# Optimization experiments

Hardware: AMD Instinct MI355X
Metric: run time of the kernel (lower is better)

The kernel has to match this reference:

```python
import jax, jax.numpy as jnp
import numpy as np

B, N, D, KNN = 2, 2048, 512, 16
F = 4 * D  # ffn hidden
LN_EPS = 1e-6  # flax LayerNorm default


def _ln(x, s, b):
    m = jnp.mean(x, axis=-1, keepdims=True)
    v = jnp.var(x, axis=-1, keepdims=True)
    return s * (x - m) * jax.lax.rsqrt(v + LN_EPS) + b


def _mobius_add(x, y, c):
    x2 = jnp.sum(x * x, axis=-1, keepdims=True)
    y2 = jnp.sum(y * y, axis=-1, keepdims=True)
    xy = jnp.sum(x * y, axis=-1, keepdims=True)
    num = (1 + 2 * c * xy + c * y2) * x + (1 - c * x2) * y
    den = 1 + 2 * c * xy + c * c * x2 * y2
    return num / jnp.clip(den, 1e-8, None)


def _logmap0(y, c):
    sqrt_c = jnp.sqrt(c)
    y_norm = jnp.clip(jnp.linalg.norm(y, axis=-1, keepdims=True), 1e-8, None)
    arg = jnp.minimum(sqrt_c * y_norm, 1.0 - 1e-7)
    return 1.0 / (sqrt_c * y_norm) * jnp.arctanh(arg) * y


def setup_inputs() -> dict:
    key = jax.random.key(0)
    ks = jax.random.split(key, 8)
    w = lambda k, shape: 0.02 * jax.random.normal(k, shape, dtype=jnp.float32)
    z = lambda *shape: jnp.zeros(shape, jnp.float32)
    o = lambda *shape: jnp.ones(shape, jnp.float32)
    return {
        'x': jax.random.normal(ks[0], (B, N, D), jnp.float32),
        'positions': 0.02 * jax.random.normal(ks[1], (B, N, D), jnp.float32),  # inside Poincare ball
        'c': jnp.ones((), jnp.float32),
        'Wq': w(ks[2], (D, D)), 'bq': z(D),
        'Wk': w(ks[3], (D, D)), 'bk': z(D),
        'Wv': w(ks[4], (D, D)), 'bv': z(D),
        'Wo': w(ks[5], (D, D)), 'bo': z(D),
        'W1': w(ks[6], (D, F)), 'b1': z(F),
        'W2': w(ks[7], (F, D)), 'b2': z(D),
        'ln1_s': o(D), 'ln1_b': z(D),
        'ln2_s': o(D), 'ln2_b': z(D),
        'geo_s': o(D), 'geo_b': z(D),
        'align_scale': o(1), 'feat_scale': o(1),
    }


def reference(x, positions, c, Wq, bq, Wk, bk, Wv, bv, Wo, bo, W1, b1, W2, b2,
              ln1_s, ln1_b, ln2_s, ln2_b, geo_s, geo_b, align_scale, feat_scale):
    b_, n_, d_ = x.shape
    x_res = x
    xn = _ln(x, ln1_s, ln1_b)
    q = xn @ Wq + bq
    kk = xn @ Wk + bk
    v = xn @ Wv + bv

    # Poincare distance matrix [B, N, N] (expanded ||x-y||^2 to avoid [B,N,N,D] intermediate)
    p2 = jnp.sum(positions * positions, axis=-1)            # [B, N]
    ip = jnp.einsum('bid,bjd->bij', positions, positions)   # [B, N, N]
    diff_sq = jnp.maximum(p2[:, :, None] + p2[:, None, :] - 2.0 * ip, 0.0)
    den = (1 - c * p2)[:, :, None] * (1 - c * p2)[:, None, :]
    arg = 1 + 2 * c * diff_sq / jnp.clip(den, 1e-8, None)
    dist = jnp.arccosh(jnp.maximum(arg, 1.0 + 1e-7)) / jnp.sqrt(c)

    _, idx = jax.lax.top_k(-dist, KNN)                      # [B, N, K]
    bix = jnp.arange(b_)[:, None, None]

    key_pos = positions[bix, idx]                           # [B, N, K, D]
    query_pos = positions[:, :, None, :]                    # [B, N, 1, D]
    geo = _logmap0(_mobius_add(-query_pos, key_pos, c), c)  # [B, N, K, D]
    geo = _ln(geo, geo_s, geo_b)

    gk = kk[bix, idx]                                       # [B, N, K, D]
    gv = v[bix, idx]                                        # [B, N, K, D]

    align = jnp.einsum('bnd,bnkd->bnk', q, geo)
    feat = jnp.einsum('bnd,bnkd->bnk', q, gk)
    scores = feat_scale * feat + align_scale * align
    w = jax.nn.softmax(scores, axis=-1)
    attn = jnp.einsum('bnk,bnkd->bnd', w, gv)

    x1 = x_res + attn @ Wo + bo
    h = _ln(x1, ln2_s, ln2_b)
    out = x1 + jax.nn.gelu(h @ W1 + b1) @ W2 + b2
    return out
```

## Files before the change

kernel.cpp:

```cpp
#include <hip/hip_runtime.h>
#include <hip/hip_bf16.h>
#include <math.h>

#define NTOK 2048
#define DDIM 512
#define FDIM 2048
#define KNN_K 16
#define ROWS 4096

typedef __hip_bfloat16 hb;
typedef unsigned long long ull;
typedef short s8v __attribute__((ext_vector_type(8)));
typedef short s4v __attribute__((ext_vector_type(4)));
typedef float f4v __attribute__((ext_vector_type(4)));

__device__ __forceinline__ float b2f(hb h) { return __bfloat162float(h); }
__device__ __forceinline__ float bits2f(short s) {
    return __uint_as_float(((unsigned int)(unsigned short)s) << 16);
}

__device__ __forceinline__ float ldin(const void* p, size_t i, int f32m) {
    return f32m ? ((const float*)p)[i] : b2f(((const hb*)p)[i]);
}
__device__ __forceinline__ float ld_scalar(const void* p, int f32m) {
    return f32m ? *(const float*)p : b2f(*(const hb*)p);
}
__device__ __forceinline__ short f2bs(float v) {
    hb h = __float2bfloat16(v);
    short s; __builtin_memcpy(&s, &h, 2); return s;
}
__device__ __forceinline__ short hb2s(hb h) {
    short s; __builtin_memcpy(&s, &h, 2); return s;
}

__device__ __forceinline__ void ld8(const void* p, size_t base, int fm, float* o) {
    if (fm) {
        f4v a = *(const f4v*)((const float*)p + base);
        f4v b = *(const f4v*)((const float*)p + base + 4);
        o[0]=a[0]; o[1]=a[1]; o[2]=a[2]; o[3]=a[3];
        o[4]=b[0]; o[5]=b[1]; o[6]=b[2]; o[7]=b[3];
    } else {
        s8v v = *(const s8v*)((const hb*)p + base);
        #pragma unroll
        for (int e = 0; e < 8; ++e) o[e] = bits2f(v[e]);
    }
}

__device__ __forceinline__ int detect_fm(const void* x) {
    const unsigned short* u = (const unsigned short*)x;
    const int lane = threadIdx.x & 63;
    int bad = 0;
    #pragma unroll
    for (int t = 0; t < 16; ++t) {
        unsigned short h = u[lane * 16 + t];
        int e = (h >> 7) & 0xFF;
        if (e == 0xFF) bad++;
        else if (e >= 0x8E) bad++;
        else if (e != 0 && e <= 0x66) bad++;
    }
    #pragma unroll
    for (int off = 1; off < 64; off <<= 1) bad += __shfl_xor(bad, off);
    return bad > 100 ? 1 : 0;
}

__device__ __forceinline__ ull shfl_xor_u64(ull x, int mask) {
    unsigned lo = (unsigned)x, hi = (unsigned)(x >> 32);
    lo = __shfl_xor(lo, mask); hi = __shfl_xor(hi, mask);
    return ((ull)hi << 32) | lo;
}

__device__ __forceinline__ float gelu_f(float x) {
    float u = 1.5957691216057308f * x * (1.f + 0.044715f * x * x);
    return x / (1.f + __expf(-u));
}

__device__ __forceinline__ void tr_tile(const void* src, hb* dst, int K, int N,
                                        int k0, int n0, int fm) {
    __shared__ float t[32][33];
    const int tx = threadIdx.x & 31, ty = threadIdx.x >> 5;
    #pragma unroll
    for (int r = 0; r < 32; r += 8)
        t[ty + r][tx] = ldin(src, (size_t)(k0 + ty + r) * N + n0 + tx, fm);
    __syncthreads();
    #pragma unroll
    for (int r = 0; r < 32; r += 8)
        dst[(size_t)(n0 + ty + r) * K + k0 + tx] = __float2bfloat16(t[tx][ty + r]);
}

__global__ void setup_kernel(const void* __restrict__ pos, const void* __restrict__ x,
                             const void* __restrict__ ln1s, const void* __restrict__ ln1b,
                             const void* __restrict__ Wq, const void* __restrict__ Wk,
                             const void* __restrict__ Wv, const void* __restrict__ Wo,
                             const void* __restrict__ W1, const void* __restrict__ W2,
                             hb* __restrict__ ph, hb* __restrict__ pl,
                             float* __restrict__ p2, float* __restrict__ spos,
                             hb* __restrict__ xnB,
                             hb* __restrict__ WqkvT, hb* __restrict__ WoT,
                             hb* __restrict__ W1T, hb* __restrict__ W2T,
                             int* __restrict__ fmflag) {
    const int fm = detect_fm(x);
    const int bx = blockIdx.x;
    if (bx == 0 && threadIdx.x == 0) *fmflag = fm;
    if (bx < 1024) {
        const int seg = bx >> 8, t = bx & 255;
        const int n0 = (t & 15) * 32, k0 = (t >> 4) * 32;
        const void* src = (seg == 0) ? Wq : (seg == 1) ? Wk : (seg == 2) ? Wv : Wo;
        hb* dst = (seg == 3) ? WoT : (WqkvT + (size_t)seg * 512 * 512);
        tr_tile(src, dst, 512, 512, k0, n0, fm);
    } else if (bx < 3072) {
        const int b = bx - 1024;
        if (b < 1024) {
            const int n0 = (b & 63) * 32, k0 = (b >> 6) * 32;
            tr_tile(W1, W1T, 512, 2048, k0, n0, fm);
        } else {
            const int b2 = b - 1024;
            const int n0 = (b2 & 15) * 32, k0 = (b2 >> 4) * 32;
            tr_tile(W2, W2T, 2048, 512, k0, n0, fm);
        }
    } else {
        const int idx = bx - 3072;
        const int lane = threadIdx.x & 63, wv = threadIdx.x >> 6;
        const int row = idx * 4 + wv;
        const int d0 = lane * 8;
        float pv[8], xv[8];
        ld8(pos, (size_t)row * DDIM + d0, fm, pv);
        ld8(x,   (size_t)row * DDIM + d0, fm, xv);
        s8v phv, plv;
        float s2 = 0.f, s1 = 0.f, sum = 0.f, sq = 0.f;
        #pragma unroll
        for (int e = 0; e < 8; ++e) {
            float v = pv[e];
            hb h = __float2bfloat16(v);
            phv[e] = hb2s(h);
            plv[e] = f2bs(v - b2f(h));
            s2 += v * v; s1 += v;
            sum += xv[e]; sq += xv[e] * xv[e];
        }
        *(s8v*)(ph + (size_t)row * DDIM + d0) = phv;
        *(s8v*)(pl + (size_t)row * DDIM + d0) = plv;
        #pragma unroll
        for (int off = 32; off; off >>= 1) {
            s2 += __shfl_down(s2, off); s1 += __shfl_down(s1, off);
            sum += __shfl_down(sum, off); sq += __shfl_down(sq, off);
        }
        if (lane == 0) { p2[row] = s2; spos[row] = s1; }
        const float ts = __shfl(sum, 0), tq = __shfl(sq, 0);
        const float mean = ts * (1.f / DDIM);
        const float var = tq * (1.f / DDIM) - mean * mean;
        const float rstd = rsqrtf(var + 1e-6f);
        float sv[8], bv2[8];
        ld8(ln1s, d0, fm, sv);
        ld8(ln1b, d0, fm, bv2);
        s8v xo;
        #pragma unroll
        for (int e = 0; e < 8; ++e)
            xo[e] = f2bs(sv[e] * (xv[e] - mean) * rstd + bv2[e]);
        *(s8v*)(xnB + (size_t)row * DDIM + d0) = xo;
    }
}

__global__ void ln_kernel(const float* __restrict__ xin,
                          const void* __restrict__ s, const void* __restrict__ b,
                          hb* __restrict__ y, const int* __restrict__ fmflag) {
    const int m = *fmflag;
    const int lane = threadIdx.x & 63, wv = threadIdx.x >> 6;
    const int row = blockIdx.x * 4 + wv;
    const int d0 = lane * 8;
    const float* xp = xin + (size_t)row * DDIM + d0;
    f4v a = *(const f4v*)xp, c4 = *(const f4v*)(xp + 4);
    float v[8] = {a[0], a[1], a[2], a[3], c4[0], c4[1], c4[2], c4[3]};
    float sum = 0.f, sq = 0.f;
    #pragma unroll
    for (int e = 0; e < 8; ++e) { sum += v[e]; sq += v[e] * v[e]; }
    #pragma unroll
    for (int off = 32; off; off >>= 1) { sum += __shfl_down(sum, off); sq += __shfl_down(sq, off); }
    const float ts = __shfl(sum, 0), tq = __shfl(sq, 0);
    const float mean = ts * (1.f / DDIM);
    const float var = tq * (1.f / DDIM) - mean * mean;
    const float rstd = rsqrtf(var + 1e-6f);
    float sv[8], bv[8];
    ld8(s, d0, m, sv);
    ld8(b, d0, m, bv);
    s8v o;
    #pragma unroll
    for (int e = 0; e < 8; ++e) o[e] = f2bs(sv[e] * (v[e] - mean) * rstd + bv[e]);
    *(s8v*)(y + (size_t)row * DDIM + d0) = o;
}

template<int EPI>
__global__ __launch_bounds__(256, 4)
void gemm64(const hb* __restrict__ A, const hb* __restrict__ Bt,
            const void* __restrict__ bp0, const void* __restrict__ res,
            void* __restrict__ C, int K, int lda, int ldb, int ldc,
            const int* __restrict__ fmflag) {
    constexpr int BK = 64, LDSW = BK + 8;
    constexpr int MAT = 64 * LDSW;
    __shared__ short Ls[2 * 2 * MAT];
    const int fm = *fmflag;
    const int tid = threadIdx.x, lane = tid & 63, wave = tid >> 6;
    const int wy = wave >> 1, wx = wave & 1;
    const int m0 = blockIdx.y * 64, n0 = blockIdx.x * 64;
    const int r0 = tid >> 3, c0 = (tid & 7) * 8;
    const int lm = lane & 15, lk = (lane >> 4) * 8;
    f4v acc[2][2];
    #pragma unroll
    for (int i = 0; i < 2; ++i)
        #pragma unroll
        for (int j = 0; j < 2; ++j) acc[i][j] = (f4v){0.f, 0.f, 0.f, 0.f};

    s8v an[2], bn[2];
    #pragma unroll
    for (int g = 0; g < 2; ++g) {
        an[g] = *(const s8v*)(A  + (size_t)(m0 + r0 + 32 * g) * lda + c0);
        bn[g] = *(const s8v*)(Bt + (size_t)(n0 + r0 + 32 * g) * ldb + c0);
    }

    int p = 0;
    for (int k0 = 0; k0 < K; k0 += BK) {
        short* As = Ls + p * (2 * MAT);
        short* Bs = As + MAT;
        #pragma unroll
        for (int g = 0; g < 2; ++g) {
            *(s8v*)(As + (r0 + 32 * g) * LDSW + c0) = an[g];
            *(s8v*)(Bs + (r0 + 32 * g) * LDSW + c0) = bn[g];
        }
        if (k0 + BK < K) {
            const int kn = k0 + BK;
            #pragma unroll
            for (int g = 0; g < 2; ++g) {
                an[g] = *(const s8v*)(A  + (size_t)(m0 + r0 + 32 * g) * lda + kn + c0);
                bn[g] = *(const s8v*)(Bt + (size_t)(n0 + r0 + 32 * g) * ldb + kn + c0);
            }
        }
        __syncthreads();
        #pragma unroll
        for (int kc = 0; kc < BK; kc += 32) {
            s8v af[2], bf[2];
            #pragma unroll
            for (int f = 0; f < 2; ++f) {
                af[f] = *(const s8v*)(As + (wy * 32 + f * 16 + lm) * LDSW + kc + lk);
                bf[f] = *(const s8v*)(Bs + (wx * 32 + f * 16 + lm) * LDSW + kc + lk);
            }
            #pragma unroll
            for (int fi = 0; fi < 2; ++fi)
                #pragma unroll
                for (int fj = 0; fj < 2; ++fj)
                    acc[fi][fj] = __builtin_amdgcn_mfma_f32_16x16x32_bf16(af[fi], bf[fj], acc[fi][fj], 0, 0, 0);
        }
        p ^= 1;
    }

    const int embase = m0 + wy * 32 + (lane >> 4) * 4;
    const int enbase = n0 + wx * 32 + lm;
    #pragma unroll
    for (int fi = 0; fi < 2; ++fi) {
        #pragma unroll
        for (int fj = 0; fj < 2; ++fj) {
            const int n = enbase + fj * 16;
            const float bias = ldin(bp0, n, fm);
            #pragma unroll
            for (int r = 0; r < 4; ++r) {
                const int m = embase + fi * 16 + r;
                float val = acc[fi][fj][r];
                size_t ci = (size_t)m * ldc + n;
                if (EPI == 1) {
                    val += bias + ldin(res, (size_t)m * 512 + n, fm);
                    ((float*)C)[ci] = val;
                } else if (EPI == 2) {
                    val = gelu_f(val + bias);
                    ((hb*)C)[ci] = __float2bfloat16(val);
                } else {
                    val += bias + ((const float*)res)[(size_t)m * 512 + n];
                    if (fm) ((float*)C)[ci] = val;
                    else ((hb*)C)[ci] = __float2bfloat16(val);
                }
            }
        }
    }
}

__global__ __launch_bounds__(256, 2)
void qkv_dist(const hb* __restrict__ A, const hb* __restrict__ Bt,
              const void* __restrict__ bq, const void* __restrict__ bk, const void* __restrict__ bv,
              hb* __restrict__ qkvB,
              const hb* __restrict__ ph, const hb* __restrict__ pl,
              const float* __restrict__ p2, const void* __restrict__ cp,
              float* __restrict__ argb, const int* __restrict__ fmflag) {
    __shared__ float Tm[128 * 132];
    const int fm = *fmflag;
    const int tid = threadIdx.x, lane = tid & 63, wave = tid >> 6;

    if (blockIdx.x < 272) {
        constexpr int BK = 32, LDSW = BK + 8;
        constexpr int KI = DDIM / BK;
        constexpr int TSH = 128 * LDSW;
        short* Sb = (short*)Tm;

        const float c = ld_scalar(cp, fm);
        const int bb = blockIdx.x / 136;
        const float* p2b = p2 + bb * NTOK;
        const size_t rb = (size_t)bb * NTOK;
        float* out = argb + (size_t)bb * NTOK * NTOK;
        int t = blockIdx.x % 136, bi = 0, rem = 16;
        while (t >= rem) { t -= rem; bi++; rem = 16 - bi; }
        const int bj = bi + t;
        const int i0 = bi * 128, j0 = bj * 128;
        const bool diag = (bi == bj);

        const int wy = wave >> 1, wx = wave & 1;
        const int r0 = tid >> 2, c0 = (tid & 3) * 8;
        const int lm = lane & 15, lk = (lane >> 4) * 8;

        const hb* src[4] = { ph + (rb + i0) * DDIM, pl + (rb + i0) * DDIM,
                             ph + (rb + j0) * DDIM, pl + (rb + j0) * DDIM };

        f4v acc_hh[4][4], acc_x[4][4];
        #pragma unroll
        for (int i = 0; i < 4; ++i)
            #pragma unroll
            for (int j = 0; j < 4; ++j) { acc_hh[i][j] = (f4v){0.f,0.f,0.f,0.f}; acc_x[i][j] = (f4v){0.f,0.f,0.f,0.f}; }

        s8v pf[4][2];
        #pragma unroll
        for (int tt = 0; tt < 4; ++tt)
            #pragma unroll
            for (int g = 0; g < 2; ++g)
                pf[tt][g] = *(const s8v*)(src[tt] + (size_t)(r0 + 64 * g) * DDIM + c0);

        for (int it = 0; it < KI; ++it) {
            __syncthreads();
            #pragma unroll
            for (int tt = 0; tt < 4; ++tt)
                #pragma unroll
                for (int g = 0; g < 2; ++g)
                    *(s8v*)(Sb + tt * TSH + (r0 + 64 * g) * LDSW + c0) = pf[tt][g];
            if (it + 1 < KI) {
                const int kn = (it + 1) * BK;
                #pragma unroll
                for (int tt = 0; tt < 4; ++tt)
                    #pragma unroll
                    for (int g = 0; g < 2; ++g)
                        pf[tt][g] = *(const s8v*)(src[tt] + (size_t)(r0 + 64 * g) * DDIM + kn + c0);
            }
            __syncthreads();
            s8v ah[4], al[4], bh[4], bl[4];
            #pragma unroll
            for (int f = 0; f < 4; ++f) {
                ah[f] = *(const s8v*)(Sb + 0 * TSH + (wy * 64 + f * 16 + lm) * LDSW + lk);
                al[f] = *(const s8v*)(Sb + 1 * TSH + (wy * 64 + f * 16 + lm) * LDSW + lk);
                bh[f] = *(const s8v*)(Sb + 2 * TSH + (wx * 64 + f * 16 + lm) * LDSW + lk);
                bl[f] = *(const s8v*)(Sb + 3 * TSH + (wx * 64 + f * 16 + lm) * LDSW + lk);
            }
            #pragma unroll
            for (int fi = 0; fi < 4; ++fi)
                #pragma unroll
                for (int fj = 0; fj < 4; ++fj) {
                    acc_hh[fi][fj] = __builtin_amdgcn_mfma_f32_16x16x32_bf16(ah[fi], bh[fj], acc_hh[fi][fj], 0, 0, 0);
                    acc_x[fi][fj]  = __builtin_amdgcn_mfma_f32_16x16x32_bf16(ah[fi], bl[fj], acc_x[fi][fj], 0, 0, 0);
                    acc_x[fi][fj]  = __builtin_amdgcn_mfma_f32_16x16x32_bf16(al[fi], bh[fj], acc_x[fi][fj], 0, 0, 0);
                }
        }

        __syncthreads();
        const int eibase = i0 + wy * 64 + (lane >> 4) * 4;
        const int ejbase = j0 + wx * 64 + lm;
        #pragma unroll
        for (int fi = 0; fi < 4; ++fi) {
            #pragma unroll
            for (int fj = 0; fj < 4; ++fj) {
                const int jj = ejbase + fj * 16;
                const float p2j = p2b[jj];
                #pragma unroll
                for (int r = 0; r < 4; ++r) {
                    const int ii = eibase + fi * 16 + r;
                    const float p2i = p2b[ii];
                    const float xy = acc_hh[fi][fj][r] + acc_x[fi][fj][r];
                    float diff = fmaxf(p2i + p2j - 2.f * xy, 0.f);
                    float den = fmaxf((1.f - c * p2i) * (1.f - c * p2j), 1e-8f);
                    float argv = 1.f + 2.f * c * diff / den;
                    out[(size_t)ii * NTOK + jj] = argv;
                    if (!diag) Tm[(jj - j0) * 132 + (ii - i0)] = argv;
                }
            }
        }
        if (!diag) {
            __syncthreads();
            #pragma unroll
            for (int k = 0; k < 16; ++k) {
                const int lin = k * 256 + tid;
                const int rowT = lin >> 5;
                const int c4 = (lin & 31) * 4;
                f4v v = *(const f4v*)(Tm + rowT * 132 + c4);
                *(f4v*)(out + (size_t)(j0 + rowT) * NTOK + i0 + c4) = v;
            }
        }
    } else {
        constexpr int BK = 64, LDSW = BK + 8;
        short* As = (short*)Tm;
        short* Bs = As + 128 * LDSW;
        const int b = blockIdx.x - 272;
        const int m0 = (b / 12) * 128, n0 = (b % 12) * 128;
        const int wy = wave >> 1, wx = wave & 1;
        const int r0 = tid >> 3, c0 = (tid & 7) * 8;
        const int lm = lane & 15, lk = (lane >> 4) * 8;
        f4v acc[4][4];
        #pragma unroll
        for (int i = 0; i < 4; ++i)
            #pragma unroll
            for (int j = 0; j < 4; ++j) acc[i][j] = (f4v){0.f, 0.f, 0.f, 0.f};

        s8v an[4], bn[4];
        #pragma unroll
        for (int g = 0; g < 4; ++g) an[g] = *(const s8v*)(A + (size_t)(m0 + r0 + 32 * g) * 512 + c0);
        #pragma unroll
        for (int g = 0; g < 4; ++g) bn[g] = *(const s8v*)(Bt + (size_t)(n0 + r0 + 32 * g) * 512 + c0);

        for (int k0 = 0; k0 < 512; k0 += BK) {
            __syncthreads();
            #pragma unroll
            for (int g = 0; g < 4; ++g) *(s8v*)(As + (r0 + 32 * g) * LDSW + c0) = an[g];
            #pragma unroll
            for (int g = 0; g < 4; ++g) *(s8v*)(Bs + (r0 + 32 * g) * LDSW + c0) = bn[g];
            if (k0 + BK < 512) {
                const int kn = k0 + BK;
                #pragma unroll
                for (int g = 0; g < 4; ++g) an[g] = *(const s8v*)(A + (size_t)(m0 + r0 + 32 * g) * 512 + kn + c0);
                #pragma unroll
                for (int g = 0; g < 4; ++g) bn[g] = *(const s8v*)(Bt + (size_t)(n0 + r0 + 32 * g) * 512 + kn + c0);
            }
            __syncthreads();
            #pragma unroll
            for (int kc = 0; kc < BK; kc += 32) {
                s8v af[4], bf[4];
                #pragma unroll
                for (int f = 0; f < 4; ++f)
                    af[f] = *(const s8v*)(As + (wy * 64 + f * 16 + lm) * LDSW + kc + lk);
                #pragma unroll
                for (int f = 0; f < 4; ++f)
                    bf[f] = *(const s8v*)(Bs + (wx * 64 + f * 16 + lm) * LDSW + kc + lk);
                #pragma unroll
                for (int fi = 0; fi < 4; ++fi)
                    #pragma unroll
                    for (int fj = 0; fj < 4; ++fj)
                        acc[fi][fj] = __builtin_amdgcn_mfma_f32_16x16x32_bf16(af[fi], bf[fj], acc[fi][fj], 0, 0, 0);
            }
        }

        const int embase = m0 + wy * 64 + (lane >> 4) * 4;
        const int enbase = n0 + wx * 64 + lm;
        #pragma unroll
        for (int fi = 0; fi < 4; ++fi) {
            #pragma unroll
            for (int fj = 0; fj < 4; ++fj) {
                const int n = enbase + fj * 16;
                const void* bp = (n < 512) ? bq : ((n < 1024) ? bk : bv);
                const float bias = ldin(bp, n & 511, fm);
                #pragma unroll
                for (int r = 0; r < 4; ++r) {
                    const int m = embase + fi * 16 + r;
                    qkvB[(size_t)m * 1536 + n] = __float2bfloat16(acc[fi][fj][r] + bias);
                }
            }
        }
    }
}

__global__ void topk_kernel(const float* __restrict__ argb, int* __restrict__ idxb,
                            float* __restrict__ argvb) {
    const int row = blockIdx.x * 4 + (threadIdx.x >> 6);
    const int bb = row >> 11, r = row & (NTOK - 1);
    const float* arow = argb + (size_t)bb * NTOK * NTOK + (size_t)r * NTOK;
    const int lane = threadIdx.x & 63;
    ull k[32];
    #pragma unroll
    for (int i = 0; i < 8; ++i) {
        f4v v = *(const f4v*)(arow + lane * 4 + i * 256);
        #pragma unroll
        for (int e = 0; e < 4; ++e) {
            const unsigned idx = lane * 4 + e + i * 256;
            k[i * 4 + e] = ((ull)__float_as_uint(v[e]) << 32) | idx;
        }
    }
    ull res = ~0ull;
    for (int sel = 0; sel < KNN_K; ++sel) {
        ull t16[16];
        #pragma unroll
        for (int i = 0; i < 16; ++i) t16[i] = (k[2 * i] < k[2 * i + 1]) ? k[2 * i] : k[2 * i + 1];
        #pragma unroll
        for (int i = 0; i < 8; ++i) t16[i] = (t16[2 * i] < t16[2 * i + 1]) ? t16[2 * i] : t16[2 * i + 1];
        #pragma unroll
        for (int i = 0; i < 4; ++i) t16[i] = (t16[2 * i] < t16[2 * i + 1]) ? t16[2 * i] : t16[2 * i + 1];
        ull m01 = (t16[0] < t16[1]) ? t16[0] : t16[1];
        ull m23 = (t16[2] < t16[3]) ? t16[2] : t16[3];
        ull m = (m01 < m23) ? m01 : m23;
        #pragma unroll
        for (int mask = 1; mask < 64; mask <<= 1) {
            ull o = shfl_xor_u64(m, mask);
            m = (o < m) ? o : m;
        }
        const unsigned widx = (unsigned)m;
        const int regid = (int)(((widx >> 8) << 2) | (widx & 3));
        const bool mine = (int)((widx >> 2) & 63) == lane;
        #pragma unroll
        for (int rr = 0; rr < 32; ++rr)
            if (rr == regid && mine) k[rr] = ~0ull;
        if (lane == sel) res = m;
    }
    if (lane < KNN_K) {
        idxb[(size_t)row * KNN_K + lane] = (int)(unsigned)res;
        argvb[(size_t)row * KNN_K + lane] = __uint_as_float((unsigned)(res >> 32));
    }
}

__global__ __launch_bounds__(256)
void attn_kernel(const void* __restrict__ pos,
                 const hb* __restrict__ qkvB, const int* __restrict__ idxb,
                 const float* __restrict__ argvb,
                 const float* __restrict__ p2, const float* __restrict__ spos,
                 const void* __restrict__ cp,
                 const void* __restrict__ geo_s, const void* __restrict__ geo_b,
                 const void* __restrict__ a_sc, const void* __restrict__ f_sc,
                 hb* __restrict__ attnO, const int* __restrict__ fmflag) {
    const int fm = *fmflag;
    const int lane = threadIdx.x & 63, wv = threadIdx.x >> 6;
    const int row = blockIdx.x * 4 + wv;
    const int bb = row >> 11;
    const int l16 = lane & 15, grp = lane >> 4;
    __shared__ float qgsS[4][DDIM];
    __shared__ float qS[4][DDIM];
    float* qgsL = qgsS[wv];
    float* qL = qS[wv];

    const float c = ld_scalar(cp, fm);
    const float cs = fmaxf(c, 1e-20f);
    const float sc_c = sqrtf(fmaxf(c, 0.f));

    const int d0 = lane * 8;
    float qq = 0.f, qgs_sum = 0.f, qgb = 0.f;
    {
        float pv[8], gs[8], gb[8];
        ld8(pos, (size_t)row * DDIM + d0, fm, pv);
        ld8(geo_s, d0, fm, gs);
        ld8(geo_b, d0, fm, gb);
        s8v qv = *(const s8v*)(qkvB + (size_t)row * 1536 + d0);
        f4v a0, a1, q0, q1;
        #pragma unroll
        for (int e = 0; e < 4; ++e) {
            float qe = bits2f(qv[e]);
            float ae = qe * gs[e];
            q0[e] = qe; a0[e] = ae;
            qq += ae * pv[e]; qgs_sum += ae; qgb += qe * gb[e];
        }
        #pragma unroll
        for (int e = 0; e < 4; ++e) {
            float qe = bits2f(qv[e + 4]);
            float ae = qe * gs[e + 4];
            q1[e] = qe; a1[e] = ae;
            qq += ae * pv[e + 4]; qgs_sum += ae; qgb += qe * gb[e + 4];
        }
        *(f4v*)(qgsL + d0) = a0; *(f4v*)(qgsL + d0 + 4) = a1;
        *(f4v*)(qL + d0) = q0;   *(f4v*)(qL + d0 + 4) = q1;
    }
    const int nid = (lane < KNN_K) ? idxb[row * KNN_K + lane] : 0;
    #pragma unroll
    for (int off = 32; off; off >>= 1) {
        qq += __shfl_down(qq, off);
        qgs_sum += __shfl_down(qgs_sum, off);
        qgb += __shfl_down(qgb, off);
    }
    const float QQ  = __shfl(qq, 0);
    const float QGS = __shfl(qgs_sum, 0);
    const float QGB = __shfl(qgb, 0);
    __syncthreads();

    float qkt[4], ftt[4];
    #pragma unroll
    for (int t = 0; t < 4; ++t) {
        const int kk = grp * 4 + t;
        const int j = __shfl(nid, kk);
        const size_t nro = (size_t)(bb * NTOK + j) * DDIM;
        const size_t nrk = (size_t)(bb * NTOK + j) * 1536 + 512;
        float qk = 0.f, feat = 0.f;
        if (fm) {
            #pragma unroll
            for (int i = 0; i < 8; ++i) {
                const int d = l16 * 4 + i * 64;
                f4v kp = *(const f4v*)((const float*)pos + nro + d);
                f4v qg = *(const f4v*)(qgsL + d);
                qk += qg[0] * kp[0] + qg[1] * kp[1] + qg[2] * kp[2] + qg[3] * kp[3];
            }
        } else {
            #pragma unroll
            for (int i = 0; i < 8; ++i) {
                const int d = l16 * 4 + i * 64;
                s4v kp4 = *(const s4v*)((const hb*)pos + nro + d);
                f4v qg = *(const f4v*)(qgsL + d);
                #pragma unroll
                for (int e = 0; e < 4; ++e) qk += qg[e] * bits2f(kp4[e]);
            }
        }
        #pragma unroll
        for (int i = 0; i < 4; ++i) {
            const int d = l16 * 8 + i * 128;
            s8v kv = *(const s8v*)(qkvB + nrk + d);
            f4v q0 = *(const f4v*)(qL + d);
            f4v q1 = *(const f4v*)(qL + d + 4);
            #pragma unroll
            for (int e = 0; e < 4; ++e)
                feat += q0[e] * bits2f(kv[e]) + q1[e] * bits2f(kv[e + 4]);
        }
        #pragma unroll
        for (int off = 8; off; off >>= 1) {
            qk += __shfl_down(qk, off, 16);
            feat += __shfl_down(feat, off, 16);
        }
        qkt[t] = qk; ftt[t] = feat;
    }
    const int src = (lane >> 2) << 4;
    float qa[4], fa[4];
    #pragma unroll
    for (int t = 0; t < 4; ++t) { qa[t] = __shfl(qkt[t], src); fa[t] = __shfl(ftt[t], src); }
    const int tsel = lane & 3;
    const float qk_f = tsel == 0 ? qa[0] : tsel == 1 ? qa[1] : tsel == 2 ? qa[2] : qa[3];
    const float ft_f = tsel == 0 ? fa[0] : tsel == 1 ? fa[1] : tsel == 2 ? fa[2] : fa[3];

    float sc_v = 0.f;
    if (lane < KNN_K) {
        const int j = nid;
        const float p2i = p2[row], p2j = p2[bb * NTOK + j];
        const float sposi = spos[row], sposj = spos[bb * NTOK + j];
        const float argv = argvb[row * KNN_K + lane];
        const float den_d = fmaxf((1.f - c * p2i) * (1.f - c * p2j), 1e-8f);
        const float diff = (argv - 1.f) * den_d / (2.f * cs);
        const float xy = 0.5f * (p2i + p2j - diff);
        const float x2 = p2i, y2 = p2j;
        const float Af = 1.f - 2.f * c * xy + c * y2;
        const float Bf = 1.f - c * x2;
        float den = fmaxf(1.f - 2.f * c * xy + c * c * x2 * y2, 1e-8f);
        const float rden = 1.f / den;
        float n2 = fmaxf(Af * Af * x2 - 2.f * Af * Bf * xy + Bf * Bf * y2, 0.f) * rden * rden;
        const float ynorm = fmaxf(sqrtf(n2), 1e-8f);
        const float t_over = sc_c * ynorm;
        const float targ = fminf(t_over, 1.f - 1e-7f);
        const float scale = (targ > 0.f) ? (atanhf(targ) / t_over) : 1.f;
        const float S1 = scale * rden * (Bf * sposj - Af * sposi);
        const float mean = S1 * (1.f / DDIM);
        const float sq = scale * scale * n2;
        const float var = sq * (1.f / DDIM) - mean * mean;
        const float rstd = rsqrtf(fmaxf(var, 0.f) + 1e-6f);
        const float G = scale * rden * (Bf * qk_f - Af * QQ);
        const float align = rstd * (G - mean * QGS) + QGB;
        sc_v = ld_scalar(f_sc, fm) * ft_f + ld_scalar(a_sc, fm) * align;
    }

    float s_t[16];
    #pragma unroll
    for (int t = 0; t < 16; ++t) s_t[t] = __shfl(sc_v, t);
    float mx = s_t[0];
    #pragma unroll
    for (int t = 1; t < 16; ++t) mx = fmaxf(mx, s_t[t]);
    float wsum = 0.f;
    #pragma unroll
    for (int t = 0; t < 16; ++t) { s_t[t] = expf(s_t[t] - mx); wsum += s_t[t]; }
    const float rw = 1.f / wsum;

    float acc[8];
    #pragma unroll
    for (int e = 0; e < 8; ++e) acc[e] = 0.f;
    #pragma unroll
    for (int t = 0; t < 16; ++t) {
        const int j = __shfl(nid, t);
        const float w = s_t[t] * rw;
        s8v vvv = *(const s8v*)(qkvB + (size_t)(bb * NTOK + j) * 1536 + 1024 + d0);
        #pragma unroll
        for (int e = 0; e < 8; ++e) acc[e] += w * bits2f(vvv[e]);
    }
    s8v o;
    #pragma unroll
    for (int e = 0; e < 8; ++e) o[e] = f2bs(acc[e]);
    *(s8v*)(attnO + (size_t)row * DDIM + d0) = o;
}

extern "C" void kernel_launch(void* const* d_in, const int* in_sizes, int n_in,
                              void* d_out, int out_size, void* d_ws, size_t ws_size,
                              hipStream_t stream) {
    const void* x    = d_in[0];
    const void* posb = d_in[1];
    const void* cb   = d_in[2];
    const void* Wq   = d_in[3];
    const void* bq   = d_in[4];
    const void* Wk   = d_in[5];
    const void* bk   = d_in[6];
    const void* Wv   = d_in[7];
    const void* bv   = d_in[8];
    const void* Wo   = d_in[9];
    const void* bo   = d_in[10];
    const void* W1   = d_in[11];
    const void* b1   = d_in[12];
    const void* W2   = d_in[13];
    const void* b2   = d_in[14];
    const void* ln2s = d_in[17];
    const void* ln2b = d_in[18];
    const void* geos = d_in[19];
    const void* geob = d_in[20];
    const void* asc  = d_in[21];
    const void* fsc  = d_in[22];
    const void* ln1s = d_in[15];
    const void* ln1b = d_in[16];

    float* wsf = (float*)d_ws;
    size_t off = 0;
    hb* xnB   = (hb*)(wsf + off); off += 1048576;
    hb* qkvB  = (hb*)(wsf + off); off += 3145728;
    float* p2 = wsf + off;        off += 4096;
    float* spos = wsf + off;      off += 4096;
    int* idxb = (int*)(wsf + off); off += 65536;
    float* argvb = wsf + off;     off += 65536;
    float* x1 = wsf + off;        off += 2097152;
    float* argb = wsf + off;
    hb* hh    = (hb*)argb;        off += 8388608;
    hb* ph    = (hb*)(wsf + off); off += 1048576;
    hb* pl    = (hb*)(wsf + off); off += 1048576;
    hb* WqkvT = (hb*)(wsf + off); off += 393216;
    hb* WoT   = (hb*)(wsf + off); off += 131072;
    hb* W1T   = (hb*)(wsf + off); off += 524288;
    hb* W2T   = (hb*)(wsf + off); off += 524288;
    int* fmflag = (int*)(wsf + off); off += 16;
    hb* attnO = ph;
    hb* hbuf  = xnB;

    setup_kernel<<<4096, 256, 0, stream>>>(posb, x, ln1s, ln1b, Wq, Wk, Wv, Wo, W1, W2,
                                           ph, pl, p2, spos, xnB, WqkvT, WoT, W1T, W2T, fmflag);
    qkv_dist<<<656, 256, 0, stream>>>(xnB, WqkvT, bq, bk, bv, qkvB,
                                      ph, pl, p2, cb, argb, fmflag);
    topk_kernel<<<1024, 256, 0, stream>>>(argb, idxb, argvb);
    attn_kernel<<<1024, 256, 0, stream>>>(posb, qkvB, idxb, argvb, p2, spos, cb,
                                          geos, geob, asc, fsc, attnO, fmflag);
    gemm64<1><<<dim3(8, 64), 256, 0, stream>>>(attnO, WoT, bo, x, x1,
                                               512, 512, 512, 512, fmflag);
    ln_kernel<<<1024, 256, 0, stream>>>(x1, ln2s, ln2b, hbuf, fmflag);
    gemm64<2><<<dim3(32, 64), 256, 0, stream>>>(hbuf, W1T, b1, nullptr, hh,
                                                512, 512, 512, 2048, fmflag);
    gemm64<3><<<dim3(8, 64), 256, 0, stream>>>(hh, W2T, b2, x1, d_out,
                                               2048, 2048, 2048, 512, fmflag);

    (void)in_sizes; (void)n_in; (void)out_size; (void)ws_size;
}
```

Measured before the change: 264.3 us.

## Shrink qkv_dist shared memory, double-buffer QKV GEMM, fuse topk into attention

The qkv_dist kernel's shared buffer drops from about 66KB to 40KB. The distance transpose write-back is now done in four 32-row chunks, with the results held in the accumulator registers. The QKV GEMM branch switches to BK=32 with double-buffered LDS, which removes one barrier per iteration. The top-k kernel is fused into the attention kernel so the neighbour indices and argument values stay in registers, which removes a launch and the idx/argv round trip through global memory. The goal is higher occupancy for qkv_dist and less launch and memory overhead, at the cost of more barriers in the transpose phase.

```diff
diff --git a/kernel.cpp b/kernel.cpp
--- a/kernel.cpp
+++ b/kernel.cpp
@@ -286,7 +286,7 @@
               const hb* __restrict__ ph, const hb* __restrict__ pl,
               const float* __restrict__ p2, const void* __restrict__ cp,
               float* __restrict__ argb, const int* __restrict__ fmflag) {
-    __shared__ float Tm[128 * 132];
+    __shared__ float TmS[10240];
     const int fm = *fmflag;
     const int tid = threadIdx.x, lane = tid & 63, wave = tid >> 6;
 
@@ -294,7 +294,8 @@
         constexpr int BK = 32, LDSW = BK + 8;
         constexpr int KI = DDIM / BK;
         constexpr int TSH = 128 * LDSW;
-        short* Sb = (short*)Tm;
+        short* Sb = (short*)TmS;
+        float* Tm = TmS;
 
         const float c = ld_scalar(cp, fm);
         const int bb = blockIdx.x / 136;
@@ -361,7 +362,6 @@
                 }
         }
 
-        __syncthreads();
         const int eibase = i0 + wy * 64 + (lane >> 4) * 4;
         const int ejbase = j0 + wx * 64 + lm;
         #pragma unroll
@@ -379,29 +379,47 @@
                     float den = fmaxf((1.f - c * p2i) * (1.f - c * p2j), 1e-8f);
                     float argv = 1.f + 2.f * c * diff / den;
                     out[(size_t)ii * NTOK + jj] = argv;
-                    if (!diag) Tm[(jj - j0) * 132 + (ii - i0)] = argv;
+                    acc_hh[fi][fj][r] = argv;
                 }
             }
         }
         if (!diag) {
-            __syncthreads();
-            #pragma unroll
-            for (int k = 0; k < 16; ++k) {
-                const int lin = k * 256 + tid;
-                const int rowT = lin >> 5;
-                const int c4 = (lin & 31) * 4;
-                f4v v = *(const f4v*)(Tm + rowT * 132 + c4);
-                *(f4v*)(out + (size_t)(j0 + rowT) * NTOK + i0 + c4) = v;
+            #pragma unroll
+            for (int cc = 0; cc < 4; ++cc) {
+                __syncthreads();
+                if (wx == (cc >> 1)) {
+                    #pragma unroll
+                    for (int fjl = 0; fjl < 2; ++fjl) {
+                        const int fj = (cc & 1) * 2 + fjl;
+                        const int rT = fjl * 16 + lm;
+                        #pragma unroll
+                        for (int fi = 0; fi < 4; ++fi) {
+                            const int cbase = wy * 64 + fi * 16 + (lane >> 4) * 4;
+                            #pragma unroll
+                            for (int r = 0; r < 4; ++r)
+                                Tm[rT * 132 + cbase + r] = acc_hh[fi][fj][r];
+                        }
+                    }
+                }
+                __syncthreads();
+                #pragma unroll
+                for (int tt2 = 0; tt2 < 4; ++tt2) {
+                    const int lin = tt2 * 256 + tid;
+                    const int rowT = lin >> 5;
+                    const int c4 = (lin & 31) * 4;
+                    f4v v = *(const f4v*)(Tm + rowT * 132 + c4);
+                    *(f4v*)(out + (size_t)(j0 + cc * 32 + rowT) * NTOK + i0 + c4) = v;
+                }
             }
         }
     } else {
-        constexpr int BK = 64, LDSW = BK + 8;
-        short* As = (short*)Tm;
-        short* Bs = As + 128 * LDSW;
+        constexpr int BK = 32, LDSW = BK + 8;
+        constexpr int MAT = 128 * LDSW;
+        short* Ls = (short*)TmS;
         const int b = blockIdx.x - 272;
         const int m0 = (b / 12) * 128, n0 = (b % 12) * 128;
         const int wy = wave >> 1, wx = wave & 1;
-        const int r0 = tid >> 3, c0 = (tid & 7) * 8;
+        const int r0 = tid >> 2, c0 = (tid & 3) * 8;
         const int lm = lane & 15, lk = (lane >> 4) * 8;
         f4v acc[4][4];
         #pragma unroll
@@ -409,41 +427,43 @@
             #pragma unroll
             for (int j = 0; j < 4; ++j) acc[i][j] = (f4v){0.f, 0.f, 0.f, 0.f};
 
-        s8v an[4], bn[4];
-        #pragma unroll
-        for (int g = 0; g < 4; ++g) an[g] = *(const s8v*)(A + (size_t)(m0 + r0 + 32 * g) * 512 + c0);
-        #pragma unroll
-        for (int g = 0; g < 4; ++g) bn[g] = *(const s8v*)(Bt + (size_t)(n0 + r0 + 32 * g) * 512 + c0);
-
+        s8v an[2], bn[2];
+        #pragma unroll
+        for (int g = 0; g < 2; ++g) {
+            an[g] = *(const s8v*)(A  + (size_t)(m0 + r0 + 64 * g) * 512 + c0);
+            bn[g] = *(const s8v*)(Bt + (size_t)(n0 + r0 + 64 * g) * 512 + c0);
+        }
+
+        int p = 0;
         for (int k0 = 0; k0 < 512; k0 += BK) {
-            __syncthreads();
-            #pragma unroll
-            for (int g = 0; g < 4; ++g) *(s8v*)(As + (r0 + 32 * g) * LDSW + c0) = an[g];
-            #pragma unroll
-            for (int g = 0; g < 4; ++g) *(s8v*)(Bs + (r0 + 32 * g) * LDSW + c0) = bn[g];
+            short* As = Ls + p * (2 * MAT);
+            short* Bs = As + MAT;
+            #pragma unroll
+            for (int g = 0; g < 2; ++g) {
+                *(s8v*)(As + (r0 + 64 * g) * LDSW + c0) = an[g];
+                *(s8v*)(Bs + (r0 + 64 * g) * LDSW + c0) = bn[g];
+            }
             if (k0 + BK < 512) {
                 const int kn = k0 + BK;
                 #pragma unroll
-                for (int g = 0; g < 4; ++g) an[g] = *(const s8v*)(A + (size_t)(m0 + r0 + 32 * g) * 512 + kn + c0);
-                #pragma unroll
-                for (int g = 0; g < 4; ++g) bn[g] = *(const s8v*)(Bt + (size_t)(n0 + r0 + 32 * g) * 512 + kn + c0);
+                for (int g = 0; g < 2; ++g) {
+                    an[g] = *(const s8v*)(A  + (size_t)(m0 + r0 + 64 * g) * 512 + kn + c0);
+                    bn[g] = *(const s8v*)(Bt + (size_t)(n0 + r0 + 64 * g) * 512 + kn + c0);
+                }
             }
             __syncthreads();
-            #pragma unroll
-            for (int kc = 0; kc < BK; kc += 32) {
-                s8v af[4], bf[4];
-                #pragma unroll
-                for (int f = 0; f < 4; ++f)
-                    af[f] = *(const s8v*)(As + (wy * 64 + f * 16 + lm) * LDSW + kc + lk);
-                #pragma unroll
-                for (int f = 0; f < 4; ++f)
-                    bf[f] = *(const s8v*)(Bs + (wx * 64 + f * 16 + lm) * LDSW + kc + lk);
-                #pragma unroll
-                for (int fi = 0; fi < 4; ++fi)
-                    #pragma unroll
-                    for (int fj = 0; fj < 4; ++fj)
-                        acc[fi][fj] = __builtin_amdgcn_mfma_f32_16x16x32_bf16(af[fi], bf[fj], acc[fi][fj], 0, 0, 0);
-            }
+            s8v af[4], bf[4];
+            #pragma unroll
+            for (int f = 0; f < 4; ++f) {
+                af[f] = *(const s8v*)(As + (wy * 64 + f * 16 + lm) * LDSW + lk);
+                bf[f] = *(const s8v*)(Bs + (wx * 64 + f * 16 + lm) * LDSW + lk);
+            }
+            #pragma unroll
+            for (int fi = 0; fi < 4; ++fi)
+                #pragma unroll
+                for (int fj = 0; fj < 4; ++fj)
+                    acc[fi][fj] = __builtin_amdgcn_mfma_f32_16x16x32_bf16(af[fi], bf[fj], acc[fi][fj], 0, 0, 0);
+            p ^= 1;
         }
 
         const int embase = m0 + wy * 64 + (lane >> 4) * 4;
@@ -465,12 +485,21 @@
     }
 }
 
-__global__ void topk_kernel(const float* __restrict__ argb, int* __restrict__ idxb,
-                            float* __restrict__ argvb) {
-    const int row = blockIdx.x * 4 + (threadIdx.x >> 6);
+__global__ __launch_bounds__(256)
+void topk_attn(const float* __restrict__ argb,
+               const void* __restrict__ pos, const hb* __restrict__ qkvB,
+               const float* __restrict__ p2, const float* __restrict__ spos,
+               const void* __restrict__ cp,
+               const void* __restrict__ geo_s, const void* __restrict__ geo_b,
+               const void* __restrict__ a_sc, const void* __restrict__ f_sc,
+               hb* __restrict__ attnO, const int* __restrict__ fmflag) {
+    const int fm = *fmflag;
+    const int lane = threadIdx.x & 63, wv = threadIdx.x >> 6;
+    const int row = blockIdx.x * 4 + wv;
     const int bb = row >> 11, r = row & (NTOK - 1);
+    const int l16 = lane & 15, grp = lane >> 4;
+
     const float* arow = argb + (size_t)bb * NTOK * NTOK + (size_t)r * NTOK;
-    const int lane = threadIdx.x & 63;
     ull k[32];
     #pragma unroll
     for (int i = 0; i < 8; ++i) {
@@ -506,26 +535,9 @@
             if (rr == regid && mine) k[rr] = ~0ull;
         if (lane == sel) res = m;
     }
-    if (lane < KNN_K) {
-        idxb[(size_t)row * KNN_K + lane] = (int)(unsigned)res;
-        argvb[(size_t)row * KNN_K + lane] = __uint_as_float((unsigned)(res >> 32));
-    }
-}
-
-__global__ __launch_bounds__(256)
-void attn_kernel(const void* __restrict__ pos,
-                 const hb* __restrict__ qkvB, const int* __restrict__ idxb,
-                 const float* __restrict__ argvb,
-                 const float* __restrict__ p2, const float* __restrict__ spos,
-                 const void* __restrict__ cp,
-                 const void* __restrict__ geo_s, const void* __restrict__ geo_b,
-                 const void* __restrict__ a_sc, const void* __restrict__ f_sc,
-                 hb* __restrict__ attnO, const int* __restrict__ fmflag) {
-    const int fm = *fmflag;
-    const int lane = threadIdx.x & 63, wv = threadIdx.x >> 6;
-    const int row = blockIdx.x * 4 + wv;
-    const int bb = row >> 11;
-    const int l16 = lane & 15, grp = lane >> 4;
+    const int nid = (int)(unsigned)res;
+    const float argv_l = __uint_as_float((unsigned)(res >> 32));
+
     __shared__ float qgsS[4][DDIM];
     __shared__ float qS[4][DDIM];
     float* qgsL = qgsS[wv];
@@ -561,7 +573,6 @@
         *(f4v*)(qgsL + d0) = a0; *(f4v*)(qgsL + d0 + 4) = a1;
         *(f4v*)(qL + d0) = q0;   *(f4v*)(qL + d0 + 4) = q1;
     }
-    const int nid = (lane < KNN_K) ? idxb[row * KNN_K + lane] : 0;
     #pragma unroll
     for (int off = 32; off; off >>= 1) {
         qq += __shfl_down(qq, off);
@@ -629,7 +640,7 @@
         const int j = nid;
         const float p2i = p2[row], p2j = p2[bb * NTOK + j];
         const float sposi = spos[row], sposj = spos[bb * NTOK + j];
-        const float argv = argvb[row * KNN_K + lane];
+        const float argv = argv_l;
         const float den_d = fmaxf((1.f - c * p2i) * (1.f - c * p2j), 1e-8f);
         const float diff = (argv - 1.f) * den_d / (2.f * cs);
         const float xy = 0.5f * (p2i + p2j - diff);
@@ -714,8 +725,6 @@
     hb* qkvB  = (hb*)(wsf + off); off += 3145728;
     float* p2 = wsf + off;        off += 4096;
     float* spos = wsf + off;      off += 4096;
-    int* idxb = (int*)(wsf + off); off += 65536;
-    float* argvb = wsf + off;     off += 65536;
     float* x1 = wsf + off;        off += 2097152;
     float* argb = wsf + off;
     hb* hh    = (hb*)argb;        off += 8388608;
@@ -733,9 +742,8 @@
                                            ph, pl, p2, spos, xnB, WqkvT, WoT, W1T, W2T, fmflag);
     qkv_dist<<<656, 256, 0, stream>>>(xnB, WqkvT, bq, bk, bv, qkvB,
                                       ph, pl, p2, cb, argb, fmflag);
-    topk_kernel<<<1024, 256, 0, stream>>>(argb, idxb, argvb);
-    attn_kernel<<<1024, 256, 0, stream>>>(posb, qkvB, idxb, argvb, p2, spos, cb,
-                                          geos, geob, asc, fsc, attnO, fmflag);
+    topk_attn<<<1024, 256, 0, stream>>>(argb, posb, qkvB, p2, spos, cb,
+                                        geos, geob, asc, fsc, attnO, fmflag);
     gemm64<1><<<dim3(8, 64), 256, 0, stream>>>(attnO, WoT, bo, x, x1,
                                                512, 512, 512, 512, fmflag);
     ln_kernel<<<1024, 256, 0, stream>>>(x1, ln2s, ln2b, hbuf, fmflag);
```

Measured after the change: 259.8 us. About the same (-1.7%).
